# Kernel optimization log

Hardware: AMD Instinct MI355X
Metric: run time of the kernel (lower is better)

Reference implementation:

```python
import jax, jax.numpy as jnp
import numpy as np
import math

B, T, D, H = 4, 1024, 1024, 16
HD = D // H  # 64
ROPE_BASE = 10000.0


def _apply_rope(q, k):
    # q, k: [B, H, T, HD]; interleaved even/odd rotation as in RotaryEmbedding
    t_len = q.shape[2]
    half = q.shape[-1] // 2
    inv_freq = 1.0 / (ROPE_BASE ** (jnp.arange(half, dtype=jnp.float32) / half))
    freqs = jnp.arange(t_len, dtype=jnp.float32)[:, None] * inv_freq  # [T, half]
    cos = jnp.cos(freqs)
    sin = jnp.sin(freqs)

    def rot(u):
        u1 = u[..., ::2]   # even lanes
        u2 = u[..., 1::2]  # odd lanes
        e = u1 * cos - u2 * sin
        o = u2 * cos + u1 * sin
        return jnp.stack([e, o], axis=-1).reshape(u.shape)

    return rot(q), rot(k)


def _split_heads(x):
    b, t, d = x.shape
    return x.reshape(b, t, H, HD).transpose(0, 2, 1, 3)  # [B,H,T,HD]


def _mha(x, Wq, bq, Wk, bk, Wv, bv, Wo, bo, mask):
    q = _split_heads(jnp.einsum('btd,ed->bte', x, Wq) + bq)
    k = _split_heads(jnp.einsum('btd,ed->bte', x, Wk) + bk)
    v = _split_heads(jnp.einsum('btd,ed->bte', x, Wv) + bv)
    q, k = _apply_rope(q, k)
    scores = jnp.einsum('bhtd,bhsd->bhts', q.astype(jnp.float32),
                        k.astype(jnp.float32)) / math.sqrt(HD)
    scores = jnp.where(mask, scores, -jnp.inf)
    attn = jax.nn.softmax(scores, axis=-1).astype(v.dtype)
    ctx = jnp.einsum('bhts,bhsd->bhtd', attn.astype(jnp.float32),
                     v.astype(jnp.float32)).astype(v.dtype)
    ctx = ctx.transpose(0, 2, 1, 3).reshape(x.shape[0], x.shape[1], D)
    z = jnp.einsum('btd,ed->bte', ctx, Wo) + bo
    return z


def setup_inputs() -> dict:
    key = jax.random.key(0)
    ks = jax.random.split(key, 9)
    s = 0.02
    inp = {
        'x':  jax.random.normal(ks[0], (B, T, D), jnp.float32),
        'Wq': jax.random.normal(ks[1], (D, D), jnp.float32) * s,
        'bq': jax.random.normal(ks[2], (D,), jnp.float32) * s,
        'Wk': jax.random.normal(ks[3], (D, D), jnp.float32) * s,
        'bk': jax.random.normal(ks[4], (D,), jnp.float32) * s,
        'Wv': jax.random.normal(ks[5], (D, D), jnp.float32) * s,
        'bv': jax.random.normal(ks[6], (D,), jnp.float32) * s,
        'Wo': jax.random.normal(ks[7], (D, D), jnp.float32) * s,
        'bo': jax.random.normal(ks[8], (D,), jnp.float32) * s,
        'mask': jnp.tril(jnp.ones((T, T), dtype=bool))[None, None],  # causal
    }
    return inp


def reference(x, Wq, bq, Wk, bk, Wv, bv, Wo, bo, mask):
    return _mha(x, Wq, bq, Wk, bk, Wv, bv, Wo, bo, mask)
```

## Files before the change

kernel.cpp:

```cpp
#include <hip/hip_runtime.h>


#define T_SEQ 1024
#define NH    16
#define HDIM  64
#define DM    1024
#define MTOK  4096

typedef __attribute__((ext_vector_type(8))) short short8;
typedef __attribute__((ext_vector_type(4))) float f32x4;
typedef unsigned short u16;

__device__ __forceinline__ u16 f2bf(float f) {
  unsigned int u = __builtin_bit_cast(unsigned int, f);
  u += 0x7fffu + ((u >> 16) & 1u);
  return (u16)(u >> 16);
}

__device__ __forceinline__ void gll16(const void* g, void* l) {
  __builtin_amdgcn_global_load_lds(
      (const __attribute__((address_space(1))) unsigned int*)(unsigned long long)(g),
      (__attribute__((address_space(3))) unsigned int*)(unsigned int)(unsigned long long)(l),
      16, 0, 0);
}

template<int N> __device__ __forceinline__ void waitvm() {
  if constexpr (N == 8)      asm volatile("s_waitcnt vmcnt(8)" ::: "memory");
  else if constexpr (N == 4) asm volatile("s_waitcnt vmcnt(4)" ::: "memory");
  else if constexpr (N == 2) asm volatile("s_waitcnt vmcnt(2)" ::: "memory");
  else                       asm volatile("s_waitcnt vmcnt(0)" ::: "memory");
}

__global__ void prep_kernel(const float* __restrict__ x,
                            const float* __restrict__ Wq, const float* __restrict__ Wk,
                            const float* __restrict__ Wv, const float* __restrict__ Wo,
                            u16* __restrict__ xb, u16* __restrict__ wall,
                            float* __restrict__ ctab, float* __restrict__ stab) {
  const int bid = blockIdx.x, tid = threadIdx.x;
  if (bid < 8192) {
    const float* src;
    u16* dst;
    int i;
    if (bid < 4096) {
      src = x; dst = xb; i = bid * 256 + tid;
    } else {
      const int w = (bid - 4096) >> 10;
      src = w == 0 ? Wq : w == 1 ? Wk : w == 2 ? Wv : Wo;
      dst = wall + (size_t)w * (DM * DM);
      i = ((bid - 4096) & 1023) * 256 + tid;
    }
    float4 f = ((const float4*)src)[i];
    unsigned long long pk = (unsigned long long)f2bf(f.x)
                          | ((unsigned long long)f2bf(f.y) << 16)
                          | ((unsigned long long)f2bf(f.z) << 32)
                          | ((unsigned long long)f2bf(f.w) << 48);
    ((unsigned long long*)dst)[i] = pk;
  } else {
    const int idx = (bid - 8192) * 256 + tid;
    const int t = idx >> 5, i = idx & 31;
    float inv = powf(10000.f, -(float)i * (1.0f / 32.0f));
    float f = (float)t * inv;
    ctab[idx] = cosf(f);
    stab[idx] = sinf(f);
  }
}

template<int BM, int BN, int AL, int BL, int MI, int NJ>
__device__ __forceinline__ void gemm_pipe4(
    const u16* __restrict__ A, const u16* __restrict__ Bw,
    int m0, int n0, u16* As, u16* Bs, f32x4 acc[MI][NJ]) {
  const int tid = threadIdx.x, lane = tid & 63, wave = tid >> 6;
  const int wr = wave >> 2, wc = wave & 3;
  const int NT = DM / 32;

  auto STG = [&](int t, int b) {
#pragma unroll
    for (int l = 0; l < AL; ++l) {
      const int idx = l * 512 + tid, r = idx >> 3, c = (idx & 7) ^ (r & 7);
      gll16(&A[(size_t)(m0 + 2 * r + (c >> 2)) * DM + t * 32 + (c & 3) * 8],
            &As[b * (BM * 32) + idx * 8]);
    }
#pragma unroll
    for (int l = 0; l < BL; ++l) {
      const int idx = l * 512 + tid, r = idx >> 3, c = (idx & 7) ^ (r & 7);
      gll16(&Bw[(size_t)(n0 + 2 * r + (c >> 2)) * DM + t * 32 + (c & 3) * 8],
            &Bs[b * (BN * 32) + idx * 8]);
    }
  };

  STG(0, 0); STG(1, 1); STG(2, 2);

  const int mrow = lane & 15, q = lane >> 4;
  int aoff[MI], boff[NJ];
#pragma unroll
  for (int i = 0; i < MI; ++i) {
    const int m = wr * (MI * 16) + i * 16 + mrow, r = m >> 1;
    const int p = (((m & 1) << 2) + q) ^ (r & 7);
    aoff[i] = r * 64 + p * 8;
  }
#pragma unroll
  for (int j = 0; j < NJ; ++j) {
    const int n = wc * (NJ * 16) + j * 16 + mrow, r = n >> 1;
    const int p = (((n & 1) << 2) + q) ^ (r & 7);
    boff[j] = r * 64 + p * 8;
  }

  for (int t = 0; t < NT; ++t) {
    if (t < NT - 2)       waitvm<2 * (AL + BL)>();
    else if (t == NT - 2) waitvm<AL + BL>();
    else                  waitvm<0>();
    asm volatile("s_waitcnt lgkmcnt(0)" ::: "memory");
    __builtin_amdgcn_s_barrier();
    if (t + 3 < NT) STG(t + 3, (t + 3) & 3);
    const int boa = (t & 3) * (BM * 32), bob = (t & 3) * (BN * 32);
    short8 af[MI], bf[NJ];
#pragma unroll
    for (int i = 0; i < MI; ++i) af[i] = *(const short8*)&As[boa + aoff[i]];
#pragma unroll
    for (int j = 0; j < NJ; ++j) bf[j] = *(const short8*)&Bs[bob + boff[j]];
#pragma unroll
    for (int i = 0; i < MI; ++i)
#pragma unroll
      for (int j = 0; j < NJ; ++j)
        acc[i][j] = __builtin_amdgcn_mfma_f32_16x16x32_bf16(af[i], bf[j], acc[i][j], 0, 0, 0);
  }
}

__global__ __launch_bounds__(512, 2) void qkv_kernel(
    const u16* __restrict__ xb, const u16* __restrict__ wqkv,
    const float* __restrict__ bq, const float* __restrict__ bk, const float* __restrict__ bv,
    const float* __restrict__ ctab, const float* __restrict__ stab,
    u16* __restrict__ qbuf, u16* __restrict__ kbuf, u16* __restrict__ vt) {
  __shared__ __align__(16) u16 As[4 * 128 * 32];
  __shared__ __align__(16) u16 Bs[4 * 384 * 32];
  const int m0 = blockIdx.y * 128;
  const int n0 = blockIdx.x * 384;
  f32x4 acc[4][6];
#pragma unroll
  for (int i = 0; i < 4; ++i)
#pragma unroll
    for (int j = 0; j < 6; ++j)
#pragma unroll
      for (int r = 0; r < 4; ++r) acc[i][j][r] = 0.f;
  gemm_pipe4<128, 384, 1, 3, 4, 6>(xb, wqkv, m0, n0, As, Bs, acc);

  const int lane = threadIdx.x & 63, wave = threadIdx.x >> 6;
  const int wr = wave >> 2, wc = wave & 3;
#pragma unroll
  for (int i = 0; i < 4; ++i) {
#pragma unroll
    for (int j = 0; j < 6; ++j) {
      const int e = n0 + wc * 96 + j * 16 + (lane & 15);
      const int mode = e >> 10;
      const float* bias = mode == 0 ? bq : (mode == 1 ? bk : bv);
      const float bval = bias[e & 1023];
      const int h = (e >> 6) & 15, hd = e & 63;
#pragma unroll
      for (int r = 0; r < 4; ++r) {
        const int m = m0 + wr * 64 + i * 16 + ((lane >> 4) * 4) + r;
        const int b = m >> 10, t = m & 1023;
        float v = acc[i][j][r] + bval;
        if (mode < 2) {
          float p = __shfl_xor(v, 1);
          const int fi = hd >> 1;
          const float cc = ctab[t * 32 + fi], ss = stab[t * 32 + fi];
          v = (hd & 1) ? (v * cc + p * ss) : (v * cc - p * ss);
          u16* dst = mode == 0 ? qbuf : kbuf;
          dst[(((size_t)(b * NH + h) * T_SEQ + t) << 6) + hd] = f2bf(v);
        } else {
          vt[(((size_t)(b * NH + h) * HDIM + hd) << 10) + t] = f2bf(v);
        }
      }
    }
  }
}

__global__ __launch_bounds__(256) void attn_kernel(
    const u16* __restrict__ qbuf, const u16* __restrict__ kbuf,
    const u16* __restrict__ vtb, u16* __restrict__ ctx) {
  __shared__ __align__(16) u16 Ks[2][64 * 64];
  __shared__ __align__(16) u16 Vs[2][64 * 64];
  __shared__ __align__(16) u16 Psm[4][16 * 64];
  const int bh = blockIdx.x;
  const int b = bh >> 4, h = bh & 15;
  const int tid = threadIdx.x, lane = tid & 63, wave = tid >> 6;
  const u16* Qp = qbuf + (size_t)bh * T_SEQ * HDIM;
  const u16* Kp = kbuf + (size_t)bh * T_SEQ * HDIM;
  const u16* Vp = vtb + (size_t)bh * HDIM * T_SEQ;
  u16* Pw = &Psm[wave][0];

  const int srow = tid >> 3;
  const int schx = ((tid & 7) ^ (srow & 7)) * 8;
  const int lx = lane & 7;

#define STG(kvt, bb)                                                            \
  do {                                                                          \
    _Pragma("unroll") for (int c = 0; c < 2; ++c) {                             \
      const int rr = c * 32 + srow;                                             \
      gll16(&Kp[(kvt) * 4096 + rr * 64 + schx], &Ks[bb][c * 2048 + tid * 8]);   \
      gll16(&Vp[(size_t)rr * T_SEQ + (kvt) * 64 + schx], &Vs[bb][c * 2048 + tid * 8]); \
    }                                                                           \
  } while (0)

  for (int phase = 0; phase < 2; ++phase) {
    const int qt = phase ? (15 - (int)blockIdx.y) : (int)blockIdx.y;
    const int q0 = qt * 64;
    const int nkv = qt + 1;
    const int qrow = q0 + wave * 16 + (lane & 15);
    const short8 qf0 = *(const short8*)&Qp[qrow * 64 + ((lane >> 4) * 8)];
    const short8 qf1 = *(const short8*)&Qp[qrow * 64 + 32 + ((lane >> 4) * 8)];

    f32x4 acc_o[4];
    float m_r[4], l_r[4];
#pragma unroll
    for (int i = 0; i < 4; ++i) {
#pragma unroll
      for (int r = 0; r < 4; ++r) acc_o[i][r] = 0.f;
      m_r[i] = -__builtin_inff();
      l_r[i] = 0.f;
    }

    __syncthreads();
    STG(0, 0);
    int cur = 0;

    for (int kvt = 0; kvt < nkv; ++kvt) {
      __syncthreads();
      if (kvt + 1 < nkv) STG(kvt + 1, cur ^ 1);

      f32x4 sacc[4];
#pragma unroll
      for (int cb = 0; cb < 4; ++cb) {
#pragma unroll
        for (int r = 0; r < 4; ++r) sacc[cb][r] = 0.f;
        const int krow = cb * 16 + (lane & 15);
        const short8 kf0 = *(const short8*)&Ks[cur][krow * 64 + (((lane >> 4) ^ lx) * 8)];
        const short8 kf1 = *(const short8*)&Ks[cur][krow * 64 + (((4 + (lane >> 4)) ^ lx) * 8)];
        sacc[cb] = __builtin_amdgcn_mfma_f32_16x16x32_bf16(qf0, kf0, sacc[cb], 0, 0, 0);
        sacc[cb] = __builtin_amdgcn_mfma_f32_16x16x32_bf16(qf1, kf1, sacc[cb], 0, 0, 0);
      }
      const int trow_base = q0 + wave * 16 + ((lane >> 4) * 4);
#pragma unroll
      for (int cb = 0; cb < 4; ++cb) {
        const int scol = kvt * 64 + cb * 16 + (lane & 15);
#pragma unroll
        for (int r = 0; r < 4; ++r) {
          float sv = sacc[cb][r] * 0.125f;
          sacc[cb][r] = (scol > trow_base + r) ? -__builtin_inff() : sv;
        }
      }
      float mt[4];
#pragma unroll
      for (int r = 0; r < 4; ++r)
        mt[r] = fmaxf(fmaxf(sacc[0][r], sacc[1][r]), fmaxf(sacc[2][r], sacc[3][r]));
#pragma unroll
      for (int off = 1; off < 16; off <<= 1)
#pragma unroll
        for (int r = 0; r < 4; ++r) mt[r] = fmaxf(mt[r], __shfl_xor(mt[r], off));
      float sf[4], lt[4];
#pragma unroll
      for (int r = 0; r < 4; ++r) {
        const float mn = fmaxf(m_r[r], mt[r]);
        sf[r] = __expf(m_r[r] - mn);
        m_r[r] = mn;
        lt[r] = 0.f;
      }
#pragma unroll
      for (int cb = 0; cb < 4; ++cb)
#pragma unroll
        for (int r = 0; r < 4; ++r) {
          const float p = __expf(sacc[cb][r] - m_r[r]);
          sacc[cb][r] = p;
          lt[r] += p;
        }
#pragma unroll
      for (int off = 1; off < 16; off <<= 1)
#pragma unroll
        for (int r = 0; r < 4; ++r) lt[r] += __shfl_xor(lt[r], off);
#pragma unroll
      for (int r = 0; r < 4; ++r) l_r[r] = l_r[r] * sf[r] + lt[r];
#pragma unroll
      for (int hb = 0; hb < 4; ++hb)
#pragma unroll
        for (int r = 0; r < 4; ++r) acc_o[hb][r] *= sf[r];

#pragma unroll
      for (int cb = 0; cb < 4; ++cb)
#pragma unroll
        for (int r = 0; r < 4; ++r) {
          const int prow = (lane >> 4) * 4 + r;
          Pw[prow * 64 + ((cb * 16 + (lane & 15)) ^ ((prow & 7) << 3))] = f2bf(sacc[cb][r]);
        }

      const int prr = lane & 15;
#pragma unroll
      for (int kc = 0; kc < 2; ++kc) {
        const short8 pf = *(const short8*)&Pw[prr * 64 + (((kc * 4 + (lane >> 4)) ^ lx) * 8)];
#pragma unroll
        for (int hb = 0; hb < 4; ++hb) {
          const int vrow = hb * 16 + (lane & 15);
          const short8 vf = *(const short8*)&Vs[cur][vrow * 64 + (((kc * 4 + (lane >> 4)) ^ lx) * 8)];
          acc_o[hb] = __builtin_amdgcn_mfma_f32_16x16x32_bf16(pf, vf, acc_o[hb], 0, 0, 0);
        }
      }
      cur ^= 1;
    }

#pragma unroll
    for (int hb = 0; hb < 4; ++hb) {
      const int hd = hb * 16 + (lane & 15);
#pragma unroll
      for (int r = 0; r < 4; ++r) {
        const int t = q0 + wave * 16 + ((lane >> 4) * 4) + r;
        const float v = acc_o[hb][r] / l_r[r];
        ctx[((size_t)(b * T_SEQ + t) * NH + h) * HDIM + hd] = f2bf(v);
      }
    }
  }
#undef STG
}

__global__ __launch_bounds__(512, 2) void oproj_kernel(
    const u16* __restrict__ ctx, const u16* __restrict__ Wob,
    const float* __restrict__ bo, float* __restrict__ out) {
  __shared__ __align__(16) u16 As[4 * 128 * 32];
  __shared__ __align__(16) u16 Bs[4 * 128 * 32];
  const int m0 = blockIdx.y * 128, n0 = blockIdx.x * 128;
  f32x4 acc[4][2];
#pragma unroll
  for (int i = 0; i < 4; ++i)
#pragma unroll
    for (int j = 0; j < 2; ++j)
#pragma unroll
      for (int r = 0; r < 4; ++r) acc[i][j][r] = 0.f;
  gemm_pipe4<128, 128, 1, 1, 4, 2>(ctx, Wob, m0, n0, As, Bs, acc);
  const int lane = threadIdx.x & 63, wave = threadIdx.x >> 6;
  const int wr = wave >> 2, wc = wave & 3;
#pragma unroll
  for (int i = 0; i < 4; ++i)
#pragma unroll
    for (int j = 0; j < 2; ++j) {
      const int e = n0 + wc * 32 + j * 16 + (lane & 15);
      const float bval = bo[e];
#pragma unroll
      for (int r = 0; r < 4; ++r) {
        const int m = m0 + wr * 64 + i * 16 + ((lane >> 4) * 4) + r;
        out[(size_t)m * DM + e] = acc[i][j][r] + bval;
      }
    }
}

extern "C" void kernel_launch(void* const* d_in, const int* in_sizes, int n_in,
                              void* d_out, int out_size, void* d_ws, size_t ws_size,
                              hipStream_t stream) {
  const float* x  = (const float*)d_in[0];
  const float* Wq = (const float*)d_in[1];
  const float* bq = (const float*)d_in[2];
  const float* Wk = (const float*)d_in[3];
  const float* bk = (const float*)d_in[4];
  const float* Wv = (const float*)d_in[5];
  const float* bv = (const float*)d_in[6];
  const float* Wo = (const float*)d_in[7];
  const float* bo = (const float*)d_in[8];

  char* w = (char*)d_ws;
  u16* xb   = (u16*)(w);
  u16* wall = (u16*)(w + (8ull << 20));
  u16* wob  = (u16*)(w + (14ull << 20));
  u16* qb   = (u16*)(w + (16ull << 20));
  u16* kb   = (u16*)(w + (24ull << 20));
  u16* vtb  = (u16*)(w + (32ull << 20));
  u16* ctxb = (u16*)(w + (40ull << 20));
  float* ctab = (float*)(w + (48ull << 20));
  float* stab = ctab + T_SEQ * 32;

  prep_kernel<<<dim3(8192 + 128), 256, 0, stream>>>(x, Wq, Wk, Wv, Wo, xb, wall, ctab, stab);
  qkv_kernel<<<dim3(3 * DM / 384, MTOK / 128), 512, 0, stream>>>(
      xb, wall, bq, bk, bv, ctab, stab, qb, kb, vtb);
  attn_kernel<<<dim3(64, 8), 256, 0, stream>>>(qb, kb, vtb, ctxb);
  oproj_kernel<<<dim3(DM / 128, MTOK / 128), 512, 0, stream>>>(ctxb, wob, bo, (float*)d_out);
}
```

Measured before the change: 118.6 us.

## Switch projection GEMMs to double-buffered smaller tiles with swizzled block order

Replaces the 4-stage global_load_lds pipeline with a simpler 2-stage double buffer synchronized by __syncthreads. Tiles become smaller: QKV uses 128x128 tiles with 256 threads, and oproj uses 64x128 tiles. Both launch a 1D grid with a block-index swizzle meant to improve L2 reuse. The goal is more blocks and higher occupancy to fill the CUs, at the cost of less prefetch depth and less reuse per tile.

New measurement: 115.4 us. 2.6% less time.

```diff
diff --git a/kernel.cpp b/kernel.cpp
--- a/kernel.cpp
+++ b/kernel.cpp
@@ -22,13 +22,6 @@
       (const __attribute__((address_space(1))) unsigned int*)(unsigned long long)(g),
       (__attribute__((address_space(3))) unsigned int*)(unsigned int)(unsigned long long)(l),
       16, 0, 0);
-}
-
-template<int N> __device__ __forceinline__ void waitvm() {
-  if constexpr (N == 8)      asm volatile("s_waitcnt vmcnt(8)" ::: "memory");
-  else if constexpr (N == 4) asm volatile("s_waitcnt vmcnt(4)" ::: "memory");
-  else if constexpr (N == 2) asm volatile("s_waitcnt vmcnt(2)" ::: "memory");
-  else                       asm volatile("s_waitcnt vmcnt(0)" ::: "memory");
 }
 
 __global__ void prep_kernel(const float* __restrict__ x,
@@ -66,53 +59,56 @@
 }
 
 template<int BM, int BN, int AL, int BL, int MI, int NJ>
-__device__ __forceinline__ void gemm_pipe4(
+__device__ __forceinline__ void gemm_dbuf(
     const u16* __restrict__ A, const u16* __restrict__ Bw,
     int m0, int n0, u16* As, u16* Bs, f32x4 acc[MI][NJ]) {
   const int tid = threadIdx.x, lane = tid & 63, wave = tid >> 6;
-  const int wr = wave >> 2, wc = wave & 3;
+  const int wr = wave >> 1, wc = wave & 1;
   const int NT = DM / 32;
 
-  auto STG = [&](int t, int b) {
-#pragma unroll
-    for (int l = 0; l < AL; ++l) {
-      const int idx = l * 512 + tid, r = idx >> 3, c = (idx & 7) ^ (r & 7);
-      gll16(&A[(size_t)(m0 + 2 * r + (c >> 2)) * DM + t * 32 + (c & 3) * 8],
-            &As[b * (BM * 32) + idx * 8]);
-    }
-#pragma unroll
-    for (int l = 0; l < BL; ++l) {
-      const int idx = l * 512 + tid, r = idx >> 3, c = (idx & 7) ^ (r & 7);
-      gll16(&Bw[(size_t)(n0 + 2 * r + (c >> 2)) * DM + t * 32 + (c & 3) * 8],
-            &Bs[b * (BN * 32) + idx * 8]);
-    }
-  };
-
-  STG(0, 0); STG(1, 1); STG(2, 2);
+  size_t aofs[AL], bofs[BL];
+  int adst[AL], bdst[BL];
+#pragma unroll
+  for (int l = 0; l < AL; ++l) {
+    const int idx = l * 256 + tid, r = idx >> 3, c = (idx & 7) ^ (r & 7);
+    aofs[l] = (size_t)(m0 + 2 * r + (c >> 2)) * DM + (c & 3) * 8;
+    adst[l] = idx * 8;
+  }
+#pragma unroll
+  for (int l = 0; l < BL; ++l) {
+    const int idx = l * 256 + tid, r = idx >> 3, c = (idx & 7) ^ (r & 7);
+    bofs[l] = (size_t)(n0 + 2 * r + (c >> 2)) * DM + (c & 3) * 8;
+    bdst[l] = idx * 8;
+  }
+
+#define STGD(t, b)                                                        \
+  do {                                                                    \
+    _Pragma("unroll") for (int l = 0; l < AL; ++l)                        \
+      gll16(&A[aofs[l] + (t) * 32], &As[(b) * (BM * 32) + adst[l]]);      \
+    _Pragma("unroll") for (int l = 0; l < BL; ++l)                        \
+      gll16(&Bw[bofs[l] + (t) * 32], &Bs[(b) * (BN * 32) + bdst[l]]);     \
+  } while (0)
 
   const int mrow = lane & 15, q = lane >> 4;
   int aoff[MI], boff[NJ];
 #pragma unroll
   for (int i = 0; i < MI; ++i) {
     const int m = wr * (MI * 16) + i * 16 + mrow, r = m >> 1;
-    const int p = (((m & 1) << 2) + q) ^ (r & 7);
+    const int p = (((m & 1) << 2) | q) ^ (r & 7);
     aoff[i] = r * 64 + p * 8;
   }
 #pragma unroll
   for (int j = 0; j < NJ; ++j) {
     const int n = wc * (NJ * 16) + j * 16 + mrow, r = n >> 1;
-    const int p = (((n & 1) << 2) + q) ^ (r & 7);
+    const int p = (((n & 1) << 2) | q) ^ (r & 7);
     boff[j] = r * 64 + p * 8;
   }
 
+  STGD(0, 0);
+  __syncthreads();
   for (int t = 0; t < NT; ++t) {
-    if (t < NT - 2)       waitvm<2 * (AL + BL)>();
-    else if (t == NT - 2) waitvm<AL + BL>();
-    else                  waitvm<0>();
-    asm volatile("s_waitcnt lgkmcnt(0)" ::: "memory");
-    __builtin_amdgcn_s_barrier();
-    if (t + 3 < NT) STG(t + 3, (t + 3) & 3);
-    const int boa = (t & 3) * (BM * 32), bob = (t & 3) * (BN * 32);
+    if (t + 1 < NT) STGD(t + 1, (t + 1) & 1);
+    const int boa = (t & 1) * (BM * 32), bob = (t & 1) * (BN * 32);
     short8 af[MI], bf[NJ];
 #pragma unroll
     for (int i = 0; i < MI; ++i) af[i] = *(const short8*)&As[boa + aoff[i]];
@@ -123,36 +119,40 @@
 #pragma unroll
       for (int j = 0; j < NJ; ++j)
         acc[i][j] = __builtin_amdgcn_mfma_f32_16x16x32_bf16(af[i], bf[j], acc[i][j], 0, 0, 0);
-  }
-}
-
-__global__ __launch_bounds__(512, 2) void qkv_kernel(
+    __syncthreads();
+  }
+#undef STGD
+}
+
+__global__ __launch_bounds__(256, 3) void qkv_kernel(
     const u16* __restrict__ xb, const u16* __restrict__ wqkv,
     const float* __restrict__ bq, const float* __restrict__ bk, const float* __restrict__ bv,
     const float* __restrict__ ctab, const float* __restrict__ stab,
     u16* __restrict__ qbuf, u16* __restrict__ kbuf, u16* __restrict__ vt) {
-  __shared__ __align__(16) u16 As[4 * 128 * 32];
-  __shared__ __align__(16) u16 Bs[4 * 384 * 32];
-  const int m0 = blockIdx.y * 128;
-  const int n0 = blockIdx.x * 384;
-  f32x4 acc[4][6];
+  __shared__ __align__(16) u16 As[2 * 128 * 32];
+  __shared__ __align__(16) u16 Bs[2 * 128 * 32];
+  const int lin = blockIdx.x;
+  const int swz = (lin & 7) * 96 + (lin >> 3);
+  const int m0 = (swz / 24) * 128;
+  const int n0 = (swz % 24) * 128;
+  f32x4 acc[4][4];
 #pragma unroll
   for (int i = 0; i < 4; ++i)
 #pragma unroll
-    for (int j = 0; j < 6; ++j)
+    for (int j = 0; j < 4; ++j)
 #pragma unroll
       for (int r = 0; r < 4; ++r) acc[i][j][r] = 0.f;
-  gemm_pipe4<128, 384, 1, 3, 4, 6>(xb, wqkv, m0, n0, As, Bs, acc);
+  gemm_dbuf<128, 128, 2, 2, 4, 4>(xb, wqkv, m0, n0, As, Bs, acc);
 
   const int lane = threadIdx.x & 63, wave = threadIdx.x >> 6;
-  const int wr = wave >> 2, wc = wave & 3;
+  const int wr = wave >> 1, wc = wave & 1;
+  const int mode = n0 >> 10;
+  const float* bias = mode == 0 ? bq : (mode == 1 ? bk : bv);
 #pragma unroll
   for (int i = 0; i < 4; ++i) {
 #pragma unroll
-    for (int j = 0; j < 6; ++j) {
-      const int e = n0 + wc * 96 + j * 16 + (lane & 15);
-      const int mode = e >> 10;
-      const float* bias = mode == 0 ? bq : (mode == 1 ? bk : bv);
+    for (int j = 0; j < 4; ++j) {
+      const int e = n0 + wc * 64 + j * 16 + (lane & 15);
       const float bval = bias[e & 1023];
       const int h = (e >> 6) & 15, hd = e & 63;
 #pragma unroll
@@ -320,31 +320,34 @@
 #undef STG
 }
 
-__global__ __launch_bounds__(512, 2) void oproj_kernel(
+__global__ __launch_bounds__(256, 2) void oproj_kernel(
     const u16* __restrict__ ctx, const u16* __restrict__ Wob,
     const float* __restrict__ bo, float* __restrict__ out) {
-  __shared__ __align__(16) u16 As[4 * 128 * 32];
-  __shared__ __align__(16) u16 Bs[4 * 128 * 32];
-  const int m0 = blockIdx.y * 128, n0 = blockIdx.x * 128;
-  f32x4 acc[4][2];
-#pragma unroll
-  for (int i = 0; i < 4; ++i)
-#pragma unroll
-    for (int j = 0; j < 2; ++j)
+  __shared__ __align__(16) u16 As[2 * 64 * 32];
+  __shared__ __align__(16) u16 Bs[2 * 128 * 32];
+  const int lin = blockIdx.x;
+  const int swz = (lin & 7) * 64 + (lin >> 3);
+  const int m0 = (swz / 8) * 64;
+  const int n0 = (swz % 8) * 128;
+  f32x4 acc[2][4];
+#pragma unroll
+  for (int i = 0; i < 2; ++i)
+#pragma unroll
+    for (int j = 0; j < 4; ++j)
 #pragma unroll
       for (int r = 0; r < 4; ++r) acc[i][j][r] = 0.f;
-  gemm_pipe4<128, 128, 1, 1, 4, 2>(ctx, Wob, m0, n0, As, Bs, acc);
+  gemm_dbuf<64, 128, 1, 2, 2, 4>(ctx, Wob, m0, n0, As, Bs, acc);
   const int lane = threadIdx.x & 63, wave = threadIdx.x >> 6;
-  const int wr = wave >> 2, wc = wave & 3;
-#pragma unroll
-  for (int i = 0; i < 4; ++i)
-#pragma unroll
-    for (int j = 0; j < 2; ++j) {
-      const int e = n0 + wc * 32 + j * 16 + (lane & 15);
+  const int wr = wave >> 1, wc = wave & 1;
+#pragma unroll
+  for (int i = 0; i < 2; ++i)
+#pragma unroll
+    for (int j = 0; j < 4; ++j) {
+      const int e = n0 + wc * 64 + j * 16 + (lane & 15);
       const float bval = bo[e];
 #pragma unroll
       for (int r = 0; r < 4; ++r) {
-        const int m = m0 + wr * 64 + i * 16 + ((lane >> 4) * 4) + r;
+        const int m = m0 + wr * 32 + i * 16 + ((lane >> 4) * 4) + r;
         out[(size_t)m * DM + e] = acc[i][j][r] + bval;
       }
     }
@@ -375,8 +378,8 @@
   float* stab = ctab + T_SEQ * 32;
 
   prep_kernel<<<dim3(8192 + 128), 256, 0, stream>>>(x, Wq, Wk, Wv, Wo, xb, wall, ctab, stab);
-  qkv_kernel<<<dim3(3 * DM / 384, MTOK / 128), 512, 0, stream>>>(
+  qkv_kernel<<<dim3(768), 256, 0, stream>>>(
       xb, wall, bq, bk, bv, ctab, stab, qb, kb, vtb);
   attn_kernel<<<dim3(64, 8), 256, 0, stream>>>(qb, kb, vtb, ctxb);
-  oproj_kernel<<<dim3(DM / 128, MTOK / 128), 512, 0, stream>>>(ctxb, wob, bo, (float*)d_out);
-}
+  oproj_kernel<<<dim3(512), 256, 0, stream>>>(ctxb, wob, bo, (float*)d_out);
+}
```
